# Kernel optimization log

Measured on AMD Instinct MI355X. Metric: run time of the kernel, lower is better.

Reference implementation:

```python
import jax, jax.numpy as jnp
import numpy as np

V = 50000
E = 800000
HIDDEN = 128
NUM_BASES = 64
D_MIN, D_MAX = 0.0, 25.0  # squared-distance range for radius=5.0


def setup_inputs() -> dict:
    key = jax.random.key(0)
    ks = jax.random.split(key, 10)
    s = 1.0 / np.sqrt(HIDDEN)
    sb = 1.0 / np.sqrt(NUM_BASES)
    return {
        "X": jax.random.normal(ks[0], (V, HIDDEN), jnp.float32),
        "R": jax.random.normal(ks[1], (V, 3), jnp.float32),
        "src": jax.random.randint(ks[2], (E,), 0, V),
        "dest": jax.random.randint(ks[3], (E,), 0, V),
        # filter-generating MLP (no bias, per nn.Linear(..., bias=False))
        "W1": jax.random.uniform(ks[4], (NUM_BASES, HIDDEN), jnp.float32, -sb, sb),
        "W2": jax.random.uniform(ks[5], (HIDDEN, HIDDEN), jnp.float32, -s, s),
        # update MLP (with bias)
        "U1": jax.random.uniform(ks[6], (HIDDEN, HIDDEN), jnp.float32, -s, s),
        "b1": jax.random.uniform(ks[7], (HIDDEN,), jnp.float32, -s, s),
        "U2": jax.random.uniform(ks[8], (HIDDEN, HIDDEN), jnp.float32, -s, s),
        "b2": jax.random.uniform(ks[9], (HIDDEN,), jnp.float32, -s, s),
    }


def _rbf(d):
    # Gaussian RBF expansion: centers linspaced over [D_MIN, D_MAX]
    centers = jnp.linspace(D_MIN, D_MAX, NUM_BASES, dtype=d.dtype)
    width = (D_MAX - D_MIN) / (NUM_BASES - 1)
    return jnp.exp(-((d[:, None] - centers) ** 2) / (2.0 * width * width))  # [E, num_bases]


def reference(X, R, src, dest, W1, W2, U1, b1, U2, b2):
    # squared pairwise distance per edge (original: .square().sum(-1), no sqrt)
    D_ij = jnp.sum((R[src] - R[dest]) ** 2, axis=-1)  # [E]
    # filter-generating network: RBF -> Linear -> ReLU -> Linear -> ReLU
    M = jax.nn.relu(_rbf(D_ij) @ W1)
    M = jax.nn.relu(M @ W2)  # [E, d_h]
    # gather-multiply-scatter: continuous-filter convolution
    H = jax.ops.segment_sum(X[src] * M, dest, num_segments=X.shape[0])  # [V, d_h]
    # update MLP (note: self.W(X) in the original is dead code, overwritten)
    out = jax.nn.relu(H @ U1 + b1) @ U2 + b2
    return out
```

## Files before the change

### kernel.cpp

```cpp
#include <hip/hip_runtime.h>
#include <hip/hip_bf16.h>
#include <hip/hip_fp16.h>

#define HIDDEN 128
#define NB 64
#define TG 2048
#define TPTS (TG + 1)
#define TMAX 32.0f
#define TINV ((float)TG / TMAX)
#define CAP 64
#define NB1 1024
#define BINCAP 24

typedef _Float16 f16;
typedef _Float16 f16x8 __attribute__((ext_vector_type(8)));
typedef float floatx4 __attribute__((ext_vector_type(4)));
typedef unsigned short ushort;
typedef unsigned int uint;

__global__ __launch_bounds__(256) void megaprep(
    const int* __restrict__ src, const int* __restrict__ dest,
    const float* __restrict__ R, float4* __restrict__ Rp,
    const float* __restrict__ X, f16* __restrict__ Xh,
    const float* __restrict__ W1, const float* __restrict__ W2,
    f16* __restrict__ Th,
    const float* __restrict__ U1, const float* __restrict__ U2,
    f16* __restrict__ U1p, f16* __restrict__ U2p,
    uint* __restrict__ staging, uint* __restrict__ cnt1,
    int E, int V, int XB, int TB, int RB, int EPB) {
    __shared__ uint smem[256 + 256 * BINCAP];
    const int b = blockIdx.x;
    const int tid = threadIdx.x;
    if (b < NB1) {
        uint* scur = smem;
        uint* sbin = smem + 256;
        scur[tid] = 0;
        __syncthreads();
        const int e0 = b * EPB;
        const int e1 = min(e0 + EPB, E);
        for (int e = e0 + tid; e < e1; e += 256) {
            const uint s = (uint)src[e];
            const uint d = (uint)dest[e];
            const uint bin = d >> 8;
            const uint k = atomicAdd(&scur[bin], 1u);
            if (k < BINCAP) sbin[bin * BINCAP + k] = s | ((d & 255u) << 16);
        }
        __syncthreads();
        uint* gslab = staging + (size_t)b * (256 * BINCAP);
        for (int i = tid; i < 256 * BINCAP; i += 256) gslab[i] = sbin[i];
        cnt1[b * 256 + tid] = scur[tid];
    } else if (b < NB1 + XB) {
        const int idx = ((b - NB1) * 256 + tid) * 8;
        if (idx < V * HIDDEN) {
            const float4 v0 = *(const float4*)(X + idx);
            const float4 v1 = *(const float4*)(X + idx + 4);
            f16x8 h;
            h[0] = (f16)v0.x; h[1] = (f16)v0.y; h[2] = (f16)v0.z; h[3] = (f16)v0.w;
            h[4] = (f16)v1.x; h[5] = (f16)v1.y; h[6] = (f16)v1.z; h[7] = (f16)v1.w;
            *(f16x8*)(Xh + idx) = h;
        }
    } else if (b < NB1 + XB + TB) {
        float* rbf = (float*)smem;
        float* m1s = (float*)smem + 128;
        const int sub = tid >> 7;
        const int c = tid & 127;
        const int g = (b - NB1 - XB) * 2 + sub;
        const float d = (float)g * (TMAX / (float)TG);
        if (c < NB) {
            const float center = 25.0f * (float)c / 63.0f;
            const float w = 25.0f / 63.0f;
            const float z = d - center;
            rbf[sub * 64 + c] = expf(-(z * z) / (2.0f * w * w));
        }
        __syncthreads();
        float acc = 0.0f;
#pragma unroll 8
        for (int k = 0; k < NB; ++k)
            acc = fmaf(rbf[sub * 64 + k], W1[k * HIDDEN + c], acc);
        m1s[sub * 128 + c] = fmaxf(acc, 0.0f);
        __syncthreads();
        float acc2 = 0.0f;
#pragma unroll 8
        for (int k = 0; k < HIDDEN; ++k)
            acc2 = fmaf(m1s[sub * 128 + k], W2[k * HIDDEN + c], acc2);
        const f16 hv = (f16)fmaxf(acc2, 0.0f);
        if (g < TG) Th[(size_t)g * 256 + 2 * c + 0] = hv;
        if (g >= 1 && g <= TG) Th[(size_t)(g - 1) * 256 + 2 * c + 1] = hv;
    } else if (b < NB1 + XB + TB + RB) {
        const int v = (b - NB1 - XB - TB) * 256 + tid;
        if (v < V) Rp[v] = make_float4(R[3 * v], R[3 * v + 1], R[3 * v + 2], 0.f);
    } else {
        const int ub = b - NB1 - XB - TB - RB;
        const int i = (ub & 63) * 256 + tid;
        const int j = i & 7;
        const int l = (i >> 3) & 63;
        const int ktct = i >> 9;
        const int kt = ktct >> 3, ct = ktct & 7;
        const int srcidx = (kt * 32 + (l >> 4) * 8 + j) * HIDDEN + ct * 16 + (l & 15);
        if (ub < 64) U1p[i] = (f16)U1[srcidx];
        else         U2p[i] = (f16)U2[srcidx];
    }
}

__global__ __launch_bounds__(256) void bucketize(
    const uint* __restrict__ staging, const uint* __restrict__ cnt1,
    ushort* __restrict__ eps, int* __restrict__ deg, int V) {
    __shared__ ushort bucket[256 * CAP];
    __shared__ uint lcur[256];
    const int r = blockIdx.x;
    const int tid = threadIdx.x;
    lcur[tid] = 0;
    __syncthreads();
    for (int b = tid; b < NB1; b += 256) {
        uint n = cnt1[b * 256 + r];
        n = min(n, (uint)BINCAP);
        const uint* seg = staging + ((size_t)b * 256 + r) * BINCAP;
        for (uint k = 0; k < n; ++k) {
            const uint e = seg[k];
            const uint dl = e >> 16;
            const uint kk = atomicAdd(&lcur[dl], 1u);
            if (kk < CAP) bucket[dl * CAP + kk] = (ushort)(e & 0xFFFFu);
        }
    }
    __syncthreads();
    const uint4* bs = (const uint4*)bucket;
    uint4* ed = (uint4*)(eps + (size_t)r * (256 * CAP));
    for (int i = tid; i < 256 * CAP / 8; i += 256) ed[i] = bs[i];
    const int d = r * 256 + tid;
    if (d < V) deg[d] = (int)min(lcur[tid], (uint)CAP);
}

__global__ __launch_bounds__(256) void gather_accum(
    const int* __restrict__ deg, const ushort* __restrict__ eps,
    const float4* __restrict__ Rp,
    const f16* __restrict__ Xh, const f16* __restrict__ Th,
    f16* __restrict__ Hf, int V) {
    const int node = blockIdx.x * 4 + (threadIdx.x >> 6);
    const int lane = threadIdx.x & 63;
    if (node >= V) return;
    const int cl = lane & 15;
    const int es = lane >> 4;
    const int dn = deg[node];
    const float4 rn = Rp[node];
    float acc[8];
#pragma unroll
    for (int i = 0; i < 8; ++i) acc[i] = 0.0f;
    const char* thb = (const char*)Th + cl * 32;
    const char* xhb = (const char*)Xh + cl * 16;
    const size_t base = (size_t)node << 6;
    for (int off = 0; off < dn; off += 64) {
        const int n = min(64, dn - off);
        int my_s = 0;
        if (lane < n) my_s = (int)eps[base + off + lane];
        const float4 rs = Rp[my_s];
        const float dx = rs.x - rn.x;
        const float dy = rs.y - rn.y;
        const float dz = rs.z - rn.z;
        const float D2 = fmaf(dx, dx, fmaf(dy, dy, dz * dz));
        const float my_u = fminf(D2 * TINV, (float)TG);
        const int nst = (n + 3) >> 2;
        for (int j = 0; j < nst; ++j) {
            const int idx = 4 * j + es;
            const int lsrc = min(idx, n - 1);
            const int s = __shfl(my_s, lsrc);
            float u = __shfl(my_u, lsrc);
            if (idx >= n) u = (float)TG;
            int g = (int)u;
            g = min(g, TG - 1);
            const float t = u - (float)g;
            const f16x8 q0 = *(const f16x8*)(thb + g * 512);
            const f16x8 q1 = *(const f16x8*)(thb + g * 512 + 16);
            const f16x8 x = *(const f16x8*)(xhb + s * 256);
#pragma unroll
            for (int i = 0; i < 4; ++i) {
                const f16 dq = (f16)(q0[2 * i + 1] - q0[2 * i]);
                const float m = fmaf((float)dq, t, (float)q0[2 * i]);
                acc[i] = fmaf(m, (float)x[i], acc[i]);
            }
#pragma unroll
            for (int i = 0; i < 4; ++i) {
                const f16 dq = (f16)(q1[2 * i + 1] - q1[2 * i]);
                const float m = fmaf((float)dq, t, (float)q1[2 * i]);
                acc[4 + i] = fmaf(m, (float)x[4 + i], acc[4 + i]);
            }
        }
    }
#pragma unroll
    for (int i = 0; i < 8; ++i) {
        acc[i] += __shfl_xor(acc[i], 16);
        acc[i] += __shfl_xor(acc[i], 32);
    }
    if (es == 0) {
        f16x8 h;
#pragma unroll
        for (int i = 0; i < 8; ++i) h[i] = (f16)acc[i];
        *(f16x8*)((char*)Hf + node * 256 + cl * 16) = h;
    }
}

__global__ __launch_bounds__(256) void node_mlp(
    const f16x8* __restrict__ Hf8, const f16x8* __restrict__ U1p,
    const float* __restrict__ b1, const f16x8* __restrict__ U2p,
    const float* __restrict__ b2, float* __restrict__ out, int V) {
    __shared__ f16 h2[32][136];
    const int tid = threadIdx.x;
    const int lane = tid & 63;
    const int w = tid >> 6;
    const int rt = w & 1;
    const int ct0 = (w >> 1) * 4;
    const int r0 = blockIdx.x * 32;
    const int lrow = lane & 15;
    const int lk = lane >> 4;

    const int arow = min(r0 + rt * 16 + lrow, V - 1);
    f16x8 a[4];
#pragma unroll
    for (int kt = 0; kt < 4; ++kt)
        a[kt] = Hf8[(size_t)arow * 16 + kt * 4 + lk];

    floatx4 acc[4];
#pragma unroll
    for (int c = 0; c < 4; ++c) acc[c] = (floatx4){0.f, 0.f, 0.f, 0.f};
#pragma unroll
    for (int c = 0; c < 4; ++c) {
        const int ct = ct0 + c;
#pragma unroll
        for (int kt = 0; kt < 4; ++kt) {
            const f16x8 bf = U1p[(kt * 8 + ct) * 64 + lane];
            acc[c] = __builtin_amdgcn_mfma_f32_16x16x32_f16(a[kt], bf, acc[c], 0, 0, 0);
        }
    }
#pragma unroll
    for (int c = 0; c < 4; ++c) {
        const int col = (ct0 + c) * 16 + lrow;
        const float bb = b1[col];
#pragma unroll
        for (int rr = 0; rr < 4; ++rr) {
            const int row = rt * 16 + lk * 4 + rr;
            h2[row][col] = (f16)fmaxf(acc[c][rr] + bb, 0.0f);
        }
    }
    __syncthreads();

#pragma unroll
    for (int kt = 0; kt < 4; ++kt)
        a[kt] = *(const f16x8*)&h2[rt * 16 + lrow][kt * 32 + lk * 8];
#pragma unroll
    for (int c = 0; c < 4; ++c) acc[c] = (floatx4){0.f, 0.f, 0.f, 0.f};
#pragma unroll
    for (int c = 0; c < 4; ++c) {
        const int ct = ct0 + c;
#pragma unroll
        for (int kt = 0; kt < 4; ++kt) {
            const f16x8 bf = U2p[(kt * 8 + ct) * 64 + lane];
            acc[c] = __builtin_amdgcn_mfma_f32_16x16x32_f16(a[kt], bf, acc[c], 0, 0, 0);
        }
    }
#pragma unroll
    for (int c = 0; c < 4; ++c) {
        const int col = (ct0 + c) * 16 + lrow;
        const float bb = b2[col];
#pragma unroll
        for (int rr = 0; rr < 4; ++rr) {
            const int row = r0 + rt * 16 + lk * 4 + rr;
            if (row < V) out[(size_t)row * HIDDEN + col] = acc[c][rr] + bb;
        }
    }
}

extern "C" void kernel_launch(void* const* d_in, const int* in_sizes, int n_in,
                              void* d_out, int out_size, void* d_ws, size_t ws_size,
                              hipStream_t stream) {
    const float* X = (const float*)d_in[0];
    const float* R = (const float*)d_in[1];
    const int* src = (const int*)d_in[2];
    const int* dest = (const int*)d_in[3];
    const float* W1 = (const float*)d_in[4];
    const float* W2 = (const float*)d_in[5];
    const float* U1 = (const float*)d_in[6];
    const float* b1 = (const float*)d_in[7];
    const float* U2 = (const float*)d_in[8];
    const float* b2 = (const float*)d_in[9];

    const int V = in_sizes[0] / HIDDEN;
    const int E = in_sizes[2];
    const int XB = (V * HIDDEN / 8 + 255) / 256;
    const int TB = (TPTS + 1) / 2;
    const int RB = (V + 255) / 256;
    const int NR = (V + 255) >> 8;
    const int EPB = (E + NB1 - 1) / NB1;

    char* base = (char*)d_ws;
    f16* Hf = (f16*)base;                       base += (size_t)V * HIDDEN * sizeof(f16);
    f16* Th = (f16*)base;                       base += (size_t)TG * 256 * sizeof(f16);
    f16* Xh = (f16*)base;                       base += (size_t)V * HIDDEN * sizeof(f16);
    ushort* eps = (ushort*)base;                base += (size_t)NR * 256 * CAP * sizeof(ushort);
    float4* Rp = (float4*)base;                 base += (size_t)V * sizeof(float4);
    f16* U1p = (f16*)base;                      base += (size_t)HIDDEN * HIDDEN * sizeof(f16);
    f16* U2p = (f16*)base;                      base += (size_t)HIDDEN * HIDDEN * sizeof(f16);
    uint* staging = (uint*)base;                base += (size_t)NB1 * 256 * BINCAP * sizeof(uint);
    uint* cnt1 = (uint*)base;                   base += (size_t)NB1 * 256 * sizeof(uint);
    int* deg = (int*)base;                      base += (size_t)NR * 256 * sizeof(int);

    megaprep<<<NB1 + XB + TB + RB + 128, 256, 0, stream>>>(
        src, dest, R, Rp, X, Xh, W1, W2, Th, U1, U2, U1p, U2p,
        staging, cnt1, E, V, XB, TB, RB, EPB);
    bucketize<<<NR, 256, 0, stream>>>(staging, cnt1, eps, deg, V);
    gather_accum<<<(V + 3) / 4, 256, 0, stream>>>(deg, eps, (const float4*)Rp,
                                                  Xh, Th, Hf, V);
    node_mlp<<<(V + 31) / 32, 256, 0, stream>>>((const f16x8*)Hf, (const f16x8*)U1p,
                                                b1, (const f16x8*)U2p, b2,
                                                (float*)d_out, V);
}
```

Before: 98.66 us.

## Use nearest-neighbor filter table lookup instead of linear interpolation

Grows the precomputed filter table from 2048 to 8192 points over the squared-distance range and stores one value per grid point, no longer an interleaved pair. The gather kernel then does a round-to-nearest lookup and a single 16-byte load per edge instead of two loads plus interpolation math, which cuts memory traffic and ALU work in the hot loop. The staging copy in the prep kernel now writes only the occupied entries of each bin, with a larger bin capacity. Nearest-neighbor sampling on a finer grid gives a different approximation error than the old interpolation, and the table takes four times as many prep blocks to build.

```diff
diff --git a/kernel.cpp b/kernel.cpp
--- a/kernel.cpp
+++ b/kernel.cpp
@@ -4,13 +4,13 @@
 
 #define HIDDEN 128
 #define NB 64
-#define TG 2048
+#define TG 8192
 #define TPTS (TG + 1)
 #define TMAX 32.0f
 #define TINV ((float)TG / TMAX)
 #define CAP 64
 #define NB1 1024
-#define BINCAP 24
+#define BINCAP 32
 
 typedef _Float16 f16;
 typedef _Float16 f16x8 __attribute__((ext_vector_type(8)));
@@ -46,9 +46,11 @@
             if (k < BINCAP) sbin[bin * BINCAP + k] = s | ((d & 255u) << 16);
         }
         __syncthreads();
-        uint* gslab = staging + (size_t)b * (256 * BINCAP);
-        for (int i = tid; i < 256 * BINCAP; i += 256) gslab[i] = sbin[i];
-        cnt1[b * 256 + tid] = scur[tid];
+        const uint n = min(scur[tid], (uint)BINCAP);
+        uint4* dst = (uint4*)(staging + ((size_t)b * 256 + tid) * BINCAP);
+        const uint4* sp = (const uint4*)(sbin + tid * BINCAP);
+        for (uint k4 = 0; k4 * 4 < n; ++k4) dst[k4] = sp[k4];
+        cnt1[b * 256 + tid] = n;
     } else if (b < NB1 + XB) {
         const int idx = ((b - NB1) * 256 + tid) * 8;
         if (idx < V * HIDDEN) {
@@ -83,9 +85,7 @@
 #pragma unroll 8
         for (int k = 0; k < HIDDEN; ++k)
             acc2 = fmaf(m1s[sub * 128 + k], W2[k * HIDDEN + c], acc2);
-        const f16 hv = (f16)fmaxf(acc2, 0.0f);
-        if (g < TG) Th[(size_t)g * 256 + 2 * c + 0] = hv;
-        if (g >= 1 && g <= TG) Th[(size_t)(g - 1) * 256 + 2 * c + 1] = hv;
+        if (g <= TG) Th[(size_t)g * 128 + c] = (f16)fmaxf(acc2, 0.0f);
     } else if (b < NB1 + XB + TB + RB) {
         const int v = (b - NB1 - XB - TB) * 256 + tid;
         if (v < V) Rp[v] = make_float4(R[3 * v], R[3 * v + 1], R[3 * v + 2], 0.f);
@@ -145,7 +145,7 @@
     float acc[8];
 #pragma unroll
     for (int i = 0; i < 8; ++i) acc[i] = 0.0f;
-    const char* thb = (const char*)Th + cl * 32;
+    const char* thb = (const char*)Th + cl * 16;
     const char* xhb = (const char*)Xh + cl * 16;
     const size_t base = (size_t)node << 6;
     for (int off = 0; off < dn; off += 64) {
@@ -157,32 +157,17 @@
         const float dy = rs.y - rn.y;
         const float dz = rs.z - rn.z;
         const float D2 = fmaf(dx, dx, fmaf(dy, dy, dz * dz));
-        const float my_u = fminf(D2 * TINV, (float)TG);
+        const int my_g = (lane < n) ? min((int)fmaf(D2, TINV, 0.5f), TG) : TG;
         const int nst = (n + 3) >> 2;
         for (int j = 0; j < nst; ++j) {
             const int idx = 4 * j + es;
-            const int lsrc = min(idx, n - 1);
-            const int s = __shfl(my_s, lsrc);
-            float u = __shfl(my_u, lsrc);
-            if (idx >= n) u = (float)TG;
-            int g = (int)u;
-            g = min(g, TG - 1);
-            const float t = u - (float)g;
-            const f16x8 q0 = *(const f16x8*)(thb + g * 512);
-            const f16x8 q1 = *(const f16x8*)(thb + g * 512 + 16);
+            const int s = __shfl(my_s, idx);
+            const int g = __shfl(my_g, idx);
+            const f16x8 m = *(const f16x8*)(thb + g * 256);
             const f16x8 x = *(const f16x8*)(xhb + s * 256);
 #pragma unroll
-            for (int i = 0; i < 4; ++i) {
-                const f16 dq = (f16)(q0[2 * i + 1] - q0[2 * i]);
-                const float m = fmaf((float)dq, t, (float)q0[2 * i]);
-                acc[i] = fmaf(m, (float)x[i], acc[i]);
-            }
-#pragma unroll
-            for (int i = 0; i < 4; ++i) {
-                const f16 dq = (f16)(q1[2 * i + 1] - q1[2 * i]);
-                const float m = fmaf((float)dq, t, (float)q1[2 * i]);
-                acc[4 + i] = fmaf(m, (float)x[4 + i], acc[4 + i]);
-            }
+            for (int i = 0; i < 8; ++i)
+                acc[i] = fmaf((float)m[i], (float)x[i], acc[i]);
         }
     }
 #pragma unroll
@@ -292,7 +277,7 @@
 
     char* base = (char*)d_ws;
     f16* Hf = (f16*)base;                       base += (size_t)V * HIDDEN * sizeof(f16);
-    f16* Th = (f16*)base;                       base += (size_t)TG * 256 * sizeof(f16);
+    f16* Th = (f16*)base;                       base += ((size_t)TPTS * 128 * sizeof(f16) + 255) & ~255;
     f16* Xh = (f16*)base;                       base += (size_t)V * HIDDEN * sizeof(f16);
     ushort* eps = (ushort*)base;                base += (size_t)NR * 256 * CAP * sizeof(ushort);
     float4* Rp = (float4*)base;                 base += (size_t)V * sizeof(float4);
```

Result: slower. 112.7 us (+14.2%).
